# Kernel optimization log

Hardware: AMD Instinct MI355X
Metric: run time of the kernel (lower is better)

The kernel has to match this reference:

```python
import jax, jax.numpy as jnp
import numpy as np

B, N, C, H = 8, 1024, 768, 12
HD = C // H
SCALE = HD ** -0.5


def setup_inputs() -> dict:
    key = jax.random.key(0)
    k1, k2, k3 = jax.random.split(key, 3)
    x = jax.random.normal(k1, (B, N, C), dtype=jnp.float32)
    # parameter init roughly matching nn.Linear default scale
    w_qkv = jax.random.normal(k2, (C, 3 * C), dtype=jnp.float32) * (C ** -0.5)
    w_out = jax.random.normal(k3, (C, C), dtype=jnp.float32) * (C ** -0.5)
    b_out = jnp.zeros((C,), dtype=jnp.float32)
    return {"x": x, "w_qkv": w_qkv, "w_out": w_out, "b_out": b_out}


def reference(x, w_qkv, w_out, b_out):
    b, n, c = x.shape
    qkv = x @ w_qkv                                   # [b, n, 3c]
    q, k, v = jnp.split(qkv, 3, axis=-1)
    # [b, n, c] -> [b, heads, n, head_dim]
    def to_heads(t):
        return t.reshape(b, n, H, HD).transpose(0, 2, 1, 3)
    q, k, v = to_heads(q), to_heads(k), to_heads(v)
    dots = jnp.einsum('bhqd,bhkd->bhqk', q, k) * SCALE  # [b, h, n, n]
    attn = jax.nn.softmax(dots, axis=-1)
    # dropout is identity in eval mode
    out = jnp.einsum('bhqk,bhkd->bhqd', attn, v)        # [b, h, n, hd]
    out = out.transpose(0, 2, 1, 3).reshape(b, n, c)
    return out @ w_out + b_out
```

## Files before the change

kernel.cpp:

```cpp
#include <hip/hip_runtime.h>
#include <stdint.h>


typedef __attribute__((ext_vector_type(8))) __bf16 bf16x8;
typedef __attribute__((ext_vector_type(4))) float f32x4;

__device__ __forceinline__ uint16_t f2bf(float f) {
    union { float f; unsigned u; } c; c.f = f;
    unsigned x = c.u;
    unsigned r = (x + 0x7FFFu + ((x >> 16) & 1u)) >> 16;
    return (uint16_t)r;
}

__device__ __forceinline__ void gload_lds16(const uint16_t* g, uint16_t* l) {
    __builtin_amdgcn_global_load_lds(
        (const __attribute__((address_space(1))) unsigned int*)g,
        (__attribute__((address_space(3))) unsigned int*)l, 16, 0, 0);
}

__global__ __launch_bounds__(256) void cvt_f32_bf16(
    const float* __restrict__ src, uint16_t* __restrict__ dst, int n) {
    int i = (blockIdx.x * 256 + threadIdx.x) * 8;
    if (i + 8 > n) return;
    float4 a = *(const float4*)(src + i);
    float4 b = *(const float4*)(src + i + 4);
    union { uint16_t u[8]; uint4 v; } o;
    o.u[0] = f2bf(a.x); o.u[1] = f2bf(a.y); o.u[2] = f2bf(a.z); o.u[3] = f2bf(a.w);
    o.u[4] = f2bf(b.x); o.u[5] = f2bf(b.y); o.u[6] = f2bf(b.z); o.u[7] = f2bf(b.w);
    *(uint4*)(dst + i) = o.v;
}

__global__ void transpose_f32_bf16(const float* __restrict__ src,
                                   uint16_t* __restrict__ dst, int R, int Cc) {
    __shared__ uint16_t tile[32][33];
    int tx = threadIdx.x, ty = threadIdx.y;
    int c0 = blockIdx.x * 32, r0 = blockIdx.y * 32;
#pragma unroll
    for (int i = 0; i < 4; i++) {
        int r = ty + i * 8;
        tile[r][tx] = f2bf(src[(size_t)(r0 + r) * Cc + c0 + tx]);
    }
    __syncthreads();
#pragma unroll
    for (int i = 0; i < 4; i++) {
        int r = ty + i * 8;
        dst[(size_t)(c0 + r) * R + r0 + tx] = tile[tx][r];
    }
}

template <int MODE>
__global__ __launch_bounds__(256) void gemm128(
    const uint16_t* __restrict__ A, const uint16_t* __restrict__ Bt,
    int Kdim, int Ncols,
    uint16_t* __restrict__ qws, uint16_t* __restrict__ kws,
    uint16_t* __restrict__ vtws,
    const float* __restrict__ bias, float* __restrict__ outp) {
    __shared__ uint16_t lA[128 * 32];
    __shared__ uint16_t lB[128 * 32];

    int tid = threadIdx.x;
    int w = tid >> 6, lane = tid & 63, quad = lane >> 4, lo = lane & 15;
    int mw = w >> 1, nw = w & 1;
    int m0 = blockIdx.y * 128;
    int n0 = blockIdx.x * 128;

    int srow = tid >> 2, skc = (tid & 3) * 8;
    const uint16_t* gA0 = A + (size_t)(m0 + srow) * Kdim + skc;
    const uint16_t* gA1 = gA0 + (size_t)64 * Kdim;
    const uint16_t* gB0 = Bt + (size_t)(n0 + srow) * Kdim + skc;
    const uint16_t* gB1 = gB0 + (size_t)64 * Kdim;
    uint16_t* lA0 = lA + tid * 8;
    uint16_t* lA1 = lA + 2048 + tid * 8;
    uint16_t* lB0 = lB + tid * 8;
    uint16_t* lB1 = lB + 2048 + tid * 8;

    f32x4 acc[4][4];
#pragma unroll
    for (int i = 0; i < 4; i++)
#pragma unroll
        for (int j = 0; j < 4; j++) acc[i][j] = (f32x4){0.f, 0.f, 0.f, 0.f};

    const uint16_t* lap = lA + ((size_t)(mw * 64 + lo) * 32) + quad * 8;
    const uint16_t* lbp = lB + ((size_t)(nw * 64 + lo) * 32) + quad * 8;

    for (int kk = 0; kk < Kdim; kk += 32) {
        gload_lds16(gA0 + kk, lA0);
        gload_lds16(gA1 + kk, lA1);
        gload_lds16(gB0 + kk, lB0);
        gload_lds16(gB1 + kk, lB1);
        __syncthreads();

        bf16x8 af[4], bfr[4];
#pragma unroll
        for (int i = 0; i < 4; i++) af[i] = *(const bf16x8*)(lap + i * 16 * 32);
#pragma unroll
        for (int j = 0; j < 4; j++) bfr[j] = *(const bf16x8*)(lbp + j * 16 * 32);
#pragma unroll
        for (int i = 0; i < 4; i++)
#pragma unroll
            for (int j = 0; j < 4; j++)
                acc[i][j] = __builtin_amdgcn_mfma_f32_16x16x32_bf16(
                    af[i], bfr[j], acc[i][j], 0, 0, 0);
        __syncthreads();
    }

    if (MODE == 0) {
        int part = n0 / 768;
        int ccb = n0 % 768 + nw * 64;
        float qsc = (part == 0) ? 0.18033688011112042f : 1.0f;
#pragma unroll
        for (int i = 0; i < 4; i++)
#pragma unroll
            for (int j = 0; j < 4; j++)
#pragma unroll
                for (int r = 0; r < 4; r++) {
                    int m = m0 + mw * 64 + i * 16 + quad * 4 + r;
                    int bidx = m >> 10, nidx = m & 1023;
                    int cc = ccb + j * 16 + lo;
                    int h = cc >> 6, d = cc & 63;
                    int bh = bidx * 12 + h;
                    uint16_t v = f2bf(acc[i][j][r] * qsc);
                    int kt = nidx >> 5, keyin = nidx & 31;
                    if (part == 0) {
                        qws[((size_t)bh * 1024 + nidx) * 64 + d] = v;
                    } else if (part == 1) {
                        int fs = ((d >> 5) << 1) | (keyin & 1);
                        int idx = ((bh << 5) + kt) * 2048 + fs * 512 +
                                  ((((d & 31) >> 3) << 4) + (keyin >> 1)) * 8 + (d & 7);
                        kws[idx] = v;
                    } else {
                        int idx = ((bh << 5) + kt) * 2048 + (d >> 4) * 512 +
                                  (((keyin >> 3) << 4) + (d & 15)) * 8 + (keyin & 7);
                        vtws[idx] = v;
                    }
                }
    } else {
#pragma unroll
        for (int i = 0; i < 4; i++)
#pragma unroll
            for (int j = 0; j < 4; j++)
#pragma unroll
                for (int r = 0; r < 4; r++) {
                    int m = m0 + mw * 64 + i * 16 + quad * 4 + r;
                    int c = n0 + nw * 64 + j * 16 + lo;
                    outp[(size_t)m * Ncols + c] = acc[i][j][r] + bias[c];
                }
    }
}

__global__ __launch_bounds__(256) void attn_kernel(
    const uint16_t* __restrict__ qws, const uint16_t* __restrict__ kws,
    const uint16_t* __restrict__ vtws, uint16_t* __restrict__ attnout) {
    int bh = blockIdx.x;
    int qt = blockIdx.y;
    int tid = threadIdx.x;
    int w = tid >> 6, lane = tid & 63, quad = lane >> 4, lo = lane & 15;
    int q0 = qt * 128 + w * 32;

    const uint16_t* Qb = qws + (size_t)bh * 65536;
    const uint16_t* Kt = kws + (size_t)bh * 65536;
    const uint16_t* Vt = vtws + (size_t)bh * 65536;

    bf16x8 aq[2][2];
#pragma unroll
    for (int rg = 0; rg < 2; rg++)
#pragma unroll
        for (int h = 0; h < 2; h++)
            aq[rg][h] = *(const bf16x8*)(Qb + (size_t)(q0 + rg * 16 + lo) * 64 + h * 32 + quad * 8);

    f32x4 oacc[2][4], ol[2];
#pragma unroll
    for (int rg = 0; rg < 2; rg++) {
        ol[rg] = (f32x4){0.f, 0.f, 0.f, 0.f};
#pragma unroll
        for (int nd = 0; nd < 4; nd++) oacc[rg][nd] = (f32x4){0.f, 0.f, 0.f, 0.f};
    }

    bf16x8 ones;
#pragma unroll
    for (int i = 0; i < 8; i++) ones[i] = (__bf16)1.0f;

    __shared__ uint16_t Kbuf[2048];
    __shared__ uint16_t Vbuf[2048];
    __shared__ uint16_t P[4][2][16][40];

    const f32x4 zero4 = (f32x4){0.f, 0.f, 0.f, 0.f};

    for (int kt = 0; kt < 32; kt++) {
        gload_lds16(Kt + kt * 2048 + tid * 8, Kbuf + tid * 8);
        gload_lds16(Vt + kt * 2048 + tid * 8, Vbuf + tid * 8);
        __syncthreads();

        bf16x8 bk[2][2], vv[4];
#pragma unroll
        for (int t = 0; t < 2; t++)
#pragma unroll
            for (int h = 0; h < 2; h++)
                bk[t][h] = *(const bf16x8*)(Kbuf + (h * 2 + t) * 512 + lane * 8);
#pragma unroll
        for (int nd = 0; nd < 4; nd++)
            vv[nd] = *(const bf16x8*)(Vbuf + nd * 512 + lane * 8);

#pragma unroll
        for (int rg = 0; rg < 2; rg++) {
            f32x4 s0 = __builtin_amdgcn_mfma_f32_16x16x32_bf16(aq[rg][0], bk[0][0], zero4, 0, 0, 0);
            s0 = __builtin_amdgcn_mfma_f32_16x16x32_bf16(aq[rg][1], bk[0][1], s0, 0, 0, 0);
            f32x4 s1 = __builtin_amdgcn_mfma_f32_16x16x32_bf16(aq[rg][0], bk[1][0], zero4, 0, 0, 0);
            s1 = __builtin_amdgcn_mfma_f32_16x16x32_bf16(aq[rg][1], bk[1][1], s1, 0, 0, 0);
#pragma unroll
            for (int r = 0; r < 4; r++) {
                union { float f; unsigned u; } u0, u1;
                u0.f = __builtin_exp2f(s0[r]);
                u1.f = __builtin_exp2f(s1[r]);
                unsigned pk = __builtin_amdgcn_perm(u1.u, u0.u, 0x07060302u);
                *(unsigned*)&P[w][rg][quad * 4 + r][2 * lo] = pk;
            }
        }

#pragma unroll
        for (int rg = 0; rg < 2; rg++) {
            bf16x8 ap = *(const bf16x8*)(&P[w][rg][lo][quad * 8]);
            ol[rg] = __builtin_amdgcn_mfma_f32_16x16x32_bf16(ap, ones, ol[rg], 0, 0, 0);
#pragma unroll
            for (int nd = 0; nd < 4; nd++)
                oacc[rg][nd] = __builtin_amdgcn_mfma_f32_16x16x32_bf16(ap, vv[nd], oacc[rg][nd], 0, 0, 0);
        }
        __syncthreads();
    }

    int b = bh / 12, hh = bh % 12;
#pragma unroll
    for (int rg = 0; rg < 2; rg++)
#pragma unroll
        for (int r = 0; r < 4; r++) {
            float inv = 1.0f / ol[rg][r];
            int n = q0 + rg * 16 + quad * 4 + r;
            size_t base = ((size_t)(b * 1024 + n)) * 768 + hh * 64;
#pragma unroll
            for (int nd = 0; nd < 4; nd++)
                attnout[base + nd * 16 + lo] = f2bf(oacc[rg][nd][r] * inv);
        }
}

extern "C" void kernel_launch(void* const* d_in, const int* in_sizes, int n_in,
                              void* d_out, int out_size, void* d_ws, size_t ws_size,
                              hipStream_t stream) {
    const float* x     = (const float*)d_in[0];
    const float* w_qkv = (const float*)d_in[1];
    const float* w_out = (const float*)d_in[2];
    const float* b_out = (const float*)d_in[3];
    float* out = (float*)d_out;

    char* ws = (char*)d_ws;
    uint16_t* xbf   = (uint16_t*)(ws);
    uint16_t* qws   = (uint16_t*)(ws + 12582912);
    uint16_t* kws   = (uint16_t*)(ws + 25165824);
    uint16_t* vtws  = (uint16_t*)(ws + 37748736);
    uint16_t* attn  = (uint16_t*)(ws + 50331648);
    uint16_t* wtqkv = (uint16_t*)(ws + 62914560);
    uint16_t* wtout = (uint16_t*)(ws + 66453504);

    cvt_f32_bf16<<<6291456 / 2048, 256, 0, stream>>>(x, xbf, 6291456);

    transpose_f32_bf16<<<dim3(2304 / 32, 768 / 32), dim3(32, 8), 0, stream>>>(w_qkv, wtqkv, 768, 2304);
    transpose_f32_bf16<<<dim3(768 / 32, 768 / 32), dim3(32, 8), 0, stream>>>(w_out, wtout, 768, 768);

    gemm128<0><<<dim3(2304 / 128, 8192 / 128), 256, 0, stream>>>(
        xbf, wtqkv, 768, 2304, qws, kws, vtws, nullptr, nullptr);

    attn_kernel<<<dim3(96, 8), 256, 0, stream>>>(qws, kws, vtws, attn);

    gemm128<1><<<dim3(768 / 128, 8192 / 128), 256, 0, stream>>>(
        attn, wtout, 768, 768, nullptr, nullptr, nullptr, b_out, out);
}
```

Baseline: 220.1 us.

## Double-buffer LDS tiles in GEMM and attention, swizzle GEMM LDS layout

Converts the GEMM and attention K/V loops to double-buffered LDS. The next tile's global-to-LDS load is issued before computing on the current tile, so load latency overlaps MFMA work. It also XOR-swizzles the GEMM's 16-byte chunk placement to cut LDS bank conflicts on fragment reads. This doubles LDS use, which may reduce occupancy. The unshown loop tail must sync properly before buffers are reused.

```diff
diff --git a/kernel.cpp b/kernel.cpp
--- a/kernel.cpp
+++ b/kernel.cpp
@@ -55,8 +55,8 @@
     uint16_t* __restrict__ qws, uint16_t* __restrict__ kws,
     uint16_t* __restrict__ vtws,
     const float* __restrict__ bias, float* __restrict__ outp) {
-    __shared__ uint16_t lA[128 * 32];
-    __shared__ uint16_t lB[128 * 32];
+    __shared__ uint16_t lA[2][4096];
+    __shared__ uint16_t lB[2][4096];
 
     int tid = threadIdx.x;
     int w = tid >> 6, lane = tid & 63, quad = lane >> 4, lo = lane & 15;
@@ -64,15 +64,12 @@
     int m0 = blockIdx.y * 128;
     int n0 = blockIdx.x * 128;
 
-    int srow = tid >> 2, skc = (tid & 3) * 8;
+    int srow = tid >> 2;
+    int skc = ((tid & 3) ^ ((tid >> 3) & 3)) * 8;
     const uint16_t* gA0 = A + (size_t)(m0 + srow) * Kdim + skc;
     const uint16_t* gA1 = gA0 + (size_t)64 * Kdim;
     const uint16_t* gB0 = Bt + (size_t)(n0 + srow) * Kdim + skc;
     const uint16_t* gB1 = gB0 + (size_t)64 * Kdim;
-    uint16_t* lA0 = lA + tid * 8;
-    uint16_t* lA1 = lA + 2048 + tid * 8;
-    uint16_t* lB0 = lB + tid * 8;
-    uint16_t* lB1 = lB + 2048 + tid * 8;
 
     f32x4 acc[4][4];
 #pragma unroll
@@ -80,21 +77,32 @@
 #pragma unroll
         for (int j = 0; j < 4; j++) acc[i][j] = (f32x4){0.f, 0.f, 0.f, 0.f};
 
-    const uint16_t* lap = lA + ((size_t)(mw * 64 + lo) * 32) + quad * 8;
-    const uint16_t* lbp = lB + ((size_t)(nw * 64 + lo) * 32) + quad * 8;
-
-    for (int kk = 0; kk < Kdim; kk += 32) {
-        gload_lds16(gA0 + kk, lA0);
-        gload_lds16(gA1 + kk, lA1);
-        gload_lds16(gB0 + kk, lB0);
-        gload_lds16(gB1 + kk, lB1);
-        __syncthreads();
+    int swz = (quad ^ ((lo >> 1) & 3)) * 8;
+    int aoff = (mw * 64 + lo) * 32 + swz;
+    int boff = (nw * 64 + lo) * 32 + swz;
+
+    const int nIter = Kdim >> 5;
+
+    gload_lds16(gA0, &lA[0][tid * 8]);
+    gload_lds16(gA1, &lA[0][2048 + tid * 8]);
+    gload_lds16(gB0, &lB[0][tid * 8]);
+    gload_lds16(gB1, &lB[0][2048 + tid * 8]);
+    __syncthreads();
+
+    for (int it = 0; it < nIter; it++) {
+        const int cur = it & 1, nxt = cur ^ 1;
+        const int kn = (it + 1 < nIter) ? (it + 1) * 32 : 0;
+
+        gload_lds16(gA0 + kn, &lA[nxt][tid * 8]);
+        gload_lds16(gA1 + kn, &lA[nxt][2048 + tid * 8]);
+        gload_lds16(gB0 + kn, &lB[nxt][tid * 8]);
+        gload_lds16(gB1 + kn, &lB[nxt][2048 + tid * 8]);
 
         bf16x8 af[4], bfr[4];
 #pragma unroll
-        for (int i = 0; i < 4; i++) af[i] = *(const bf16x8*)(lap + i * 16 * 32);
-#pragma unroll
-        for (int j = 0; j < 4; j++) bfr[j] = *(const bf16x8*)(lbp + j * 16 * 32);
+        for (int i = 0; i < 4; i++) af[i] = *(const bf16x8*)(&lA[cur][aoff + i * 512]);
+#pragma unroll
+        for (int j = 0; j < 4; j++) bfr[j] = *(const bf16x8*)(&lB[cur][boff + j * 512]);
 #pragma unroll
         for (int i = 0; i < 4; i++)
 #pragma unroll
@@ -180,26 +188,32 @@
 #pragma unroll
     for (int i = 0; i < 8; i++) ones[i] = (__bf16)1.0f;
 
-    __shared__ uint16_t Kbuf[2048];
-    __shared__ uint16_t Vbuf[2048];
+    __shared__ uint16_t Kbuf[2][2048];
+    __shared__ uint16_t Vbuf[2][2048];
     __shared__ uint16_t P[4][2][16][40];
 
     const f32x4 zero4 = (f32x4){0.f, 0.f, 0.f, 0.f};
 
+    gload_lds16(Kt + tid * 8, &Kbuf[0][tid * 8]);
+    gload_lds16(Vt + tid * 8, &Vbuf[0][tid * 8]);
+    __syncthreads();
+
     for (int kt = 0; kt < 32; kt++) {
-        gload_lds16(Kt + kt * 2048 + tid * 8, Kbuf + tid * 8);
-        gload_lds16(Vt + kt * 2048 + tid * 8, Vbuf + tid * 8);
-        __syncthreads();
+        const int cur = kt & 1, nxt = cur ^ 1;
+        const int ktn = (kt + 1) & 31;
+
+        gload_lds16(Kt + ktn * 2048 + tid * 8, &Kbuf[nxt][tid * 8]);
+        gload_lds16(Vt + ktn * 2048 + tid * 8, &Vbuf[nxt][tid * 8]);
 
         bf16x8 bk[2][2], vv[4];
 #pragma unroll
         for (int t = 0; t < 2; t++)
 #pragma unroll
             for (int h = 0; h < 2; h++)
-                bk[t][h] = *(const bf16x8*)(Kbuf + (h * 2 + t) * 512 + lane * 8);
+                bk[t][h] = *(const bf16x8*)(&Kbuf[cur][(h * 2 + t) * 512 + lane * 8]);
 #pragma unroll
         for (int nd = 0; nd < 4; nd++)
-            vv[nd] = *(const bf16x8*)(Vbuf + nd * 512 + lane * 8);
+            vv[nd] = *(const bf16x8*)(&Vbuf[cur][nd * 512 + lane * 8]);
 
 #pragma unroll
         for (int rg = 0; rg < 2; rg++) {
```

Measured after the change: 220.7 us. No clear change (+0.3%).
